# Kernel optimization log

Hardware: AMD Instinct MI355X
Metric: run time of the kernel (lower is better)

## Reference

```python
import jax, jax.numpy as jnp
import numpy as np

ALPHA, GAMMA = 0.25, 2.0
ACCEPT, REJECT = 0.5, 0.4
CLF_W, REG_W = 1.0, 50.0
SL1_R = 9.0  # reg_smooth_l1_loss_scaling_factor
EPS = 1e-4


def _calc_iou(a, b):
    # a: [A,4] anchors in yxyx ; b: [M,4] gt boxes in xyxy (as in original code)
    ay1, ax1, ay2, ax2 = a[:, 0], a[:, 1], a[:, 2], a[:, 3]
    bx1, by1, bx2, by2 = b[:, 0], b[:, 1], b[:, 2], b[:, 3]
    iw = jnp.clip(jnp.minimum(ax2[:, None], bx2) - jnp.maximum(ax1[:, None], bx1), 0.0)
    ih = jnp.clip(jnp.minimum(ay2[:, None], by2) - jnp.maximum(ay1[:, None], by1), 0.0)
    inter = iw * ih  # [A, M]
    aarea = ((ax2 - ax1) * (ay2 - ay1))[:, None]
    barea = (bx2 - bx1) * (by2 - by1)
    union = jnp.clip(aarea + barea - inter, 1e-8)
    return inter / union


def _single_image(clf, reg, ann, anchors, a_cx, a_cy, a_w, a_h):
    # clf: [A,C], reg: [A,4], ann: [M,5] (x1,y1,x2,y2,label; label=-1 => pad)
    clf = jnp.clip(clf, EPS, 1.0 - EPS)
    labels = ann[:, 4]
    valid = labels != -1.0  # [M]
    boxes = ann[:, :4]
    iou = _calc_iou(anchors, boxes)               # [A, M]
    iou = jnp.where(valid[None, :], iou, -1.0)    # invalid GT never matches
    iou_max = iou.max(axis=-1)                    # [A]
    iou_arg = iou.argmax(axis=-1)                 # [A]
    matched = iou_max > ACCEPT
    unmatched = iou_max < REJECT
    num_matched = matched.sum()
    # classification targets: -1 (ignore) by default, 0 for unmatched, one-hot for matched
    gt_lbl = labels[iou_arg].astype(jnp.int32) - 1  # [A]
    one_hot = jax.nn.one_hot(gt_lbl, clf.shape[-1], dtype=clf.dtype)
    tgt = jnp.where(matched[:, None], one_hot,
                    jnp.where(unmatched[:, None], 0.0, -1.0))
    pos = ALPHA * (1.0 - clf) ** GAMMA * (-jnp.log(clf))
    neg = (1.0 - ALPHA) * clf ** GAMMA * (-jnp.log(1.0 - clf))
    clf_losses = jnp.where(tgt == 1.0, pos, neg)
    clf_losses = jnp.where(tgt == -1.0, 0.0, clf_losses)
    clf_loss = clf_losses.sum() / jnp.maximum(1, num_matched).astype(clf.dtype)
    gb = boxes[iou_arg]  # [A,4] xyxy
    gw_raw = gb[:, 2] - gb[:, 0]
    gh_raw = gb[:, 3] - gb[:, 1]
    gcx = gb[:, 0] + 0.5 * gw_raw
    gcy = gb[:, 1] + 0.5 * gh_raw
    gw = jnp.clip(gw_raw, 1.0)
    gh = jnp.clip(gh_raw, 1.0)
    reg_t = jnp.stack(((gcy - a_cy) / a_h,
                       (gcx - a_cx) / a_w,
                       jnp.log(gh / a_h),
                       jnp.log(gw / a_w)), axis=-1)  # [A,4] (dy,dx,dh,dw)
    d = jnp.abs(SL1_R * (reg - reg_t))
    sl1 = jnp.where(d < 1.0, 0.5 * d * d, d - 0.5)
    sl1 = jnp.where(matched[:, None], sl1, 0.0)
    denom = jnp.maximum(1, 4 * num_matched).astype(clf.dtype)
    reg_loss = jnp.where(num_matched > 0, sl1.sum() / denom, 0.0)
    return clf_loss, reg_loss


def setup_inputs() -> dict:
    key = jax.random.key(0)
    ks = jax.random.split(key, 12)
    B, A, C, M = 8, 49104, 90, 32
    clf = jax.random.uniform(ks[0], (B, A, C), jnp.float32)
    reg = jax.random.normal(ks[1], (B, A, 4), jnp.float32)
    # anchors in yxyx, all with positive width/height
    y1 = jax.random.uniform(ks[2], (A,)) * 480.0
    x1 = jax.random.uniform(ks[3], (A,)) * 480.0
    ah = jax.random.uniform(ks[4], (A,)) * 120.0 + 8.0
    aw = jax.random.uniform(ks[5], (A,)) * 120.0 + 8.0
    anchors = jnp.stack([y1, x1, y1 + ah, x1 + aw], axis=-1)[None].astype(jnp.float32)
    # annotations: xyxy boxes + label in [1, C]; ~half padded with label -1
    bx1 = jax.random.uniform(ks[6], (B, M)) * 400.0
    by1 = jax.random.uniform(ks[7], (B, M)) * 400.0
    bw = jax.random.uniform(ks[8], (B, M)) * 100.0 + 20.0
    bh = jax.random.uniform(ks[9], (B, M)) * 100.0 + 20.0
    lbl = jax.random.randint(ks[10], (B, M), 1, C + 1).astype(jnp.float32)
    lbl = jnp.where(jax.random.uniform(ks[11], (B, M)) < 0.6, lbl, -1.0)
    ann = jnp.stack([bx1, by1, bx1 + bw, by1 + bh, lbl], axis=-1).astype(jnp.float32)
    return {"classifications": clf, "regressions": reg, "anchors": anchors, "annotations": ann}


def reference(classifications, regressions, anchors, annotations):
    anc = anchors.squeeze()  # [A,4] yxyx
    a_w = anc[:, 3] - anc[:, 1]
    a_h = anc[:, 2] - anc[:, 0]
    a_cx = anc[:, 1] + 0.5 * a_w
    a_cy = anc[:, 0] + 0.5 * a_h
    clf = jnp.clip(classifications, EPS, 1.0 - EPS)
    clf_l, reg_l = jax.vmap(_single_image, in_axes=(0, 0, 0, None, None, None, None, None))(
        clf, regressions, annotations, anc, a_cx, a_cy, a_w, a_h)
    return CLF_W * clf_l.mean(), REG_W * reg_l.mean()
```

## Files before the change

kernel.cpp:

```cpp
#include <hip/hip_runtime.h>


namespace {
constexpr int B_N = 8;
constexpr int A_N = 49104;
constexpr int C_N = 90;
constexpr int M_N = 32;
constexpr float EPSF   = 1e-4f;
constexpr float ACCEPT = 0.5f;
constexpr float REJECT = 0.4f;
constexpr float SL1R   = 9.0f;
constexpr float CLFW   = 1.0f;
constexpr float REGW   = 50.0f;
constexpr float LN2    = 0.69314718055994530942f;

constexpr int APB = 256;
constexpr int NBX = (A_N + APB - 1) / APB;

__device__ __forceinline__ float clampx(float x) {
    return __builtin_amdgcn_fmed3f(x, EPSF, 1.0f - EPSF);
}
__device__ __forceinline__ float neg_term(float x) {
    x = clampx(x);
    return 0.75f * x * x * (-__logf(1.0f - x));
}
__device__ __forceinline__ float pos_term(float x) {
    x = clampx(x);
    float o = 1.0f - x;
    return 0.25f * o * o * (-__logf(x));
}
}

__global__ void fused_kernel(const float* __restrict__ anchors,
                             const float* __restrict__ reg,
                             const float* __restrict__ ann,
                             const float* __restrict__ clf,
                             float4* __restrict__ part)
{
    __shared__ float sann[M_N * 5];
    __shared__ int   s_match[APB];
    __shared__ int   s_ign[APB];
    __shared__ int   s_nm, s_ni;
    __shared__ float sred[4][4];

    const int b   = blockIdx.y;
    const int a0  = blockIdx.x * APB;
    const int tid = threadIdx.x;
    if (tid < M_N * 5) sann[tid] = ann[b * M_N * 5 + tid];
    if (tid == 0) { s_nm = 0; s_ni = 0; }
    __syncthreads();

    float cnt  = 0.0f;
    float rsum = 0.0f;
    float corr = 0.0f;
    const int i = a0 + tid;

    if (i < A_N) {
        const float4 av = ((const float4*)anchors)[i];
        const float ay1 = av.x, ax1 = av.y, ay2 = av.z, ax2 = av.w;
        const float aw = ax2 - ax1, ah = ay2 - ay1;
        const float aarea = aw * ah;

        float best = -3.4e38f;
        int   arg  = 0;
        #pragma unroll 8
        for (int j = 0; j < M_N; ++j) {
            const float bx1 = sann[j*5+0], by1 = sann[j*5+1];
            const float bx2 = sann[j*5+2], by2 = sann[j*5+3];
            const float lb  = sann[j*5+4];
            float iw = fminf(ax2, bx2) - fmaxf(ax1, bx1); iw = fmaxf(iw, 0.0f);
            float ih = fminf(ay2, by2) - fmaxf(ay1, by1); ih = fmaxf(ih, 0.0f);
            const float inter = iw * ih;
            const float barea = (bx2 - bx1) * (by2 - by1);
            const float uni   = fmaxf(aarea + barea - inter, 1e-8f);
            float iou = inter / uni;
            if (lb == -1.0f) iou = -1.0f;
            if (iou > best) { best = iou; arg = j; }
        }

        const bool matched   = best > ACCEPT;
        const bool unmatched = best < REJECT;

        if (matched) {
            const int s = (int)sann[arg*5+4] - 1;
            cnt = 1.0f;
            const int slot = atomicAdd(&s_nm, 1);
            s_match[slot] = (tid << 8) | s;
            const float bx1 = sann[arg*5+0], by1 = sann[arg*5+1];
            const float bx2 = sann[arg*5+2], by2 = sann[arg*5+3];
            const float gwr = bx2 - bx1, ghr = by2 - by1;
            const float gcx = bx1 + 0.5f * gwr, gcy = by1 + 0.5f * ghr;
            const float gw  = fmaxf(gwr, 1.0f), gh = fmaxf(ghr, 1.0f);
            const float acx = ax1 + 0.5f * aw, acy = ay1 + 0.5f * ah;
            const float t0 = (gcy - acy) / ah;
            const float t1 = (gcx - acx) / aw;
            const float t2 = __logf(gh / ah);
            const float t3 = __logf(gw / aw);
            const float4 rv = ((const float4*)reg)[b * A_N + i];
            float d;
            d = fabsf(SL1R * (rv.x - t0)); rsum += (d < 1.0f) ? 0.5f*d*d : d - 0.5f;
            d = fabsf(SL1R * (rv.y - t1)); rsum += (d < 1.0f) ? 0.5f*d*d : d - 0.5f;
            d = fabsf(SL1R * (rv.z - t2)); rsum += (d < 1.0f) ? 0.5f*d*d : d - 0.5f;
            d = fabsf(SL1R * (rv.w - t3)); rsum += (d < 1.0f) ? 0.5f*d*d : d - 0.5f;
        } else if (!unmatched) {
            const int slot = atomicAdd(&s_ni, 1);
            s_ign[slot] = tid;
        }
    }
    __syncthreads();

    const int nA  = min(APB, A_N - a0);
    const int nF4 = nA * C_N / 4;
    const float4* __restrict__ p =
        (const float4*)(clf + ((size_t)b * A_N + a0) * C_N);

    float S = 0.0f;

    auto w4 = [](float4 v) -> float {
        float s = 0.0f;
        const float x0 = clampx(v.x), x1 = clampx(v.y);
        const float x2 = clampx(v.z), x3 = clampx(v.w);
        s = fmaf(x0 * x0, __log2f(1.0f - x0), s);
        s = fmaf(x1 * x1, __log2f(1.0f - x1), s);
        s = fmaf(x2 * x2, __log2f(1.0f - x2), s);
        s = fmaf(x3 * x3, __log2f(1.0f - x3), s);
        return s;
    };

    int f = tid;
    #pragma unroll 1
    for (; f + 768 < nF4; f += 1024) {
        const float4 v0 = p[f];
        const float4 v1 = p[f + 256];
        const float4 v2 = p[f + 512];
        const float4 v3 = p[f + 768];
        S += w4(v0) + w4(v1) + w4(v2) + w4(v3);
    }
    for (; f < nF4; f += 256) S += w4(p[f]);

    const int nm = s_nm, ni = s_ni;
    for (int k = tid; k < nm; k += 256) {
        const int packed = s_match[k];
        const int a  = packed >> 8;
        const int sc = packed & 0xFF;
        const float x = clf[((size_t)b * A_N + a0 + a) * C_N + sc];
        corr += pos_term(x) - neg_term(x);
    }
    const int wid  = tid >> 6;
    const int lane = tid & 63;
    for (int e = wid; e < ni; e += 4) {
        const int a = s_ign[e];
        const float2* __restrict__ r2 =
            (const float2*)(clf + ((size_t)b * A_N + a0 + a) * C_N);
        if (lane < 45) {
            const float2 u = r2[lane];
            corr -= neg_term(u.x) + neg_term(u.y);
        }
    }

    #pragma unroll
    for (int off = 32; off > 0; off >>= 1) {
        cnt  += __shfl_down(cnt,  off);
        rsum += __shfl_down(rsum, off);
        S    += __shfl_down(S,    off);
        corr += __shfl_down(corr, off);
    }
    if (lane == 0) {
        sred[wid][0] = cnt; sred[wid][1] = rsum;
        sred[wid][2] = S;   sred[wid][3] = corr;
    }
    __syncthreads();
    if (tid == 0) {
        float c = 0.f, r = 0.f, ss = 0.f, k = 0.f;
        #pragma unroll
        for (int w = 0; w < 4; ++w) {
            c += sred[w][0]; r += sred[w][1]; ss += sred[w][2]; k += sred[w][3];
        }
        part[b * NBX + blockIdx.x] = make_float4(c, r, ss, k);
    }
}

__global__ void finalize_kernel(const float4* __restrict__ part,
                                float*        __restrict__ out)
{
    __shared__ float s_cnt[B_N], s_rsum[B_N], s_S[B_N], s_corr[B_N];
    const int tid = threadIdx.x;
    const int b   = tid >> 5;
    const int j   = tid & 31;

    float cnt = 0.f, rsum = 0.f, S = 0.f, corr = 0.f;
    #pragma unroll
    for (int k = 0; k < NBX / 32; ++k) {
        const float4 m = part[b * NBX + j + 32 * k];
        cnt += m.x; rsum += m.y; S += m.z; corr += m.w;
    }
    #pragma unroll
    for (int off = 16; off > 0; off >>= 1) {
        cnt  += __shfl_down(cnt,  off, 32);
        rsum += __shfl_down(rsum, off, 32);
        S    += __shfl_down(S,    off, 32);
        corr += __shfl_down(corr, off, 32);
    }
    if (j == 0) { s_cnt[b] = cnt; s_rsum[b] = rsum; s_S[b] = S; s_corr[b] = corr; }
    __syncthreads();
    if (tid == 0) {
        float cl = 0.0f, rl = 0.0f;
        #pragma unroll
        for (int bb = 0; bb < B_N; ++bb) {
            const float n = s_cnt[bb];
            const float clf_total = -0.75f * LN2 * s_S[bb] + s_corr[bb];
            cl += clf_total / fmaxf(1.0f, n);
            if (n > 0.0f) rl += s_rsum[bb] / (4.0f * n);
        }
        out[0] = CLFW * (cl / (float)B_N);
        out[1] = REGW * (rl / (float)B_N);
    }
}

extern "C" void kernel_launch(void* const* d_in, const int* in_sizes, int n_in,
                              void* d_out, int out_size, void* d_ws, size_t ws_size,
                              hipStream_t stream) {
    const float* clf     = (const float*)d_in[0];
    const float* reg     = (const float*)d_in[1];
    const float* anchors = (const float*)d_in[2];
    const float* ann     = (const float*)d_in[3];
    float*  out  = (float*)d_out;
    float4* part = (float4*)d_ws;

    {
        dim3 grid(NBX, B_N);
        fused_kernel<<<grid, 256, 0, stream>>>(anchors, reg, ann, clf, part);
    }
    finalize_kernel<<<1, 256, 0, stream>>>(part, out);
}
```

Baseline: 215.2 us.

## Split dense classification stream into separate block range from matching blocks

The dense per-element focal-loss sum over the classification tensor moves into its own set of 512 blocks per image, each streaming a contiguous chunk with 8 loads in flight and two accumulators. The IoU matching blocks now only compute counts, regression loss and sparse corrections. This lets the bandwidth-bound stream run without waiting on the IoU matching, and the stream blocks avoid the matching work and shared-memory setup. In exchange there are more partial results to reduce, and launch bounds are set for occupancy.

Result: no change. 215.2 us (+0.0%).

```diff
diff --git a/kernel.cpp b/kernel.cpp
--- a/kernel.cpp
+++ b/kernel.cpp
@@ -14,8 +14,14 @@
 constexpr float REGW   = 50.0f;
 constexpr float LN2    = 0.69314718055994530942f;
 
-constexpr int APB = 256;
-constexpr int NBX = (A_N + APB - 1) / APB;
+constexpr int APB  = 256;
+constexpr int MBX  = (A_N + APB - 1) / APB;
+constexpr int SBX  = 512;
+constexpr int IMG_F4 = A_N * C_N / 4;
+constexpr int CHUNK  = (IMG_F4 + SBX - 1) / SBX;
+
+constexpr int MSLOTS = MBX * B_N;
+constexpr int SSLOT0 = MSLOTS;
 
 __device__ __forceinline__ float clampx(float x) {
     return __builtin_amdgcn_fmed3f(x, EPSF, 1.0f - EPSF);
@@ -31,11 +37,12 @@
 }
 }
 
-__global__ void fused_kernel(const float* __restrict__ anchors,
-                             const float* __restrict__ reg,
-                             const float* __restrict__ ann,
-                             const float* __restrict__ clf,
-                             float4* __restrict__ part)
+__global__ void __launch_bounds__(256, 8)
+fused_kernel(const float* __restrict__ anchors,
+             const float* __restrict__ reg,
+             const float* __restrict__ ann,
+             const float* __restrict__ clf,
+             float4* __restrict__ part)
 {
     __shared__ float sann[M_N * 5];
     __shared__ int   s_match[APB];
@@ -44,8 +51,59 @@
     __shared__ float sred[4][4];
 
     const int b   = blockIdx.y;
-    const int a0  = blockIdx.x * APB;
     const int tid = threadIdx.x;
+    const int wid  = tid >> 6;
+    const int lane = tid & 63;
+
+    if (blockIdx.x >= MBX) {
+        const int sx    = blockIdx.x - MBX;
+        const int fbase = sx * CHUNK;
+        const int n     = min(CHUNK, IMG_F4 - fbase);
+        const float4* __restrict__ p =
+            (const float4*)(clf + (size_t)b * (A_N * C_N)) + fbase;
+
+        auto w4 = [](float4 v) -> float {
+            float s = 0.0f;
+            const float x0 = clampx(v.x), x1 = clampx(v.y);
+            const float x2 = clampx(v.z), x3 = clampx(v.w);
+            s = fmaf(x0 * x0, __log2f(1.0f - x0), s);
+            s = fmaf(x1 * x1, __log2f(1.0f - x1), s);
+            s = fmaf(x2 * x2, __log2f(1.0f - x2), s);
+            s = fmaf(x3 * x3, __log2f(1.0f - x3), s);
+            return s;
+        };
+
+        float S0 = 0.0f, S1 = 0.0f;
+        int f = tid;
+        #pragma unroll 1
+        for (; f + 1792 < n; f += 2048) {
+            const float4 v0 = p[f];
+            const float4 v1 = p[f + 256];
+            const float4 v2 = p[f + 512];
+            const float4 v3 = p[f + 768];
+            const float4 v4 = p[f + 1024];
+            const float4 v5 = p[f + 1280];
+            const float4 v6 = p[f + 1536];
+            const float4 v7 = p[f + 1792];
+            S0 += w4(v0) + w4(v2) + w4(v4) + w4(v6);
+            S1 += w4(v1) + w4(v3) + w4(v5) + w4(v7);
+        }
+        #pragma unroll 1
+        for (; f < n; f += 256) S0 += w4(p[f]);
+        float S = S0 + S1;
+
+        #pragma unroll
+        for (int off = 32; off > 0; off >>= 1) S += __shfl_down(S, off);
+        if (lane == 0) sred[wid][0] = S;
+        __syncthreads();
+        if (tid == 0) {
+            part[SSLOT0 + b * SBX + sx] =
+                make_float4(0.f, 0.f, sred[0][0] + sred[1][0] + sred[2][0] + sred[3][0], 0.f);
+        }
+        return;
+    }
+
+    const int a0 = blockIdx.x * APB;
     if (tid < M_N * 5) sann[tid] = ann[b * M_N * 5 + tid];
     if (tid == 0) { s_nm = 0; s_ni = 0; }
     __syncthreads();
@@ -109,35 +167,6 @@
     }
     __syncthreads();
 
-    const int nA  = min(APB, A_N - a0);
-    const int nF4 = nA * C_N / 4;
-    const float4* __restrict__ p =
-        (const float4*)(clf + ((size_t)b * A_N + a0) * C_N);
-
-    float S = 0.0f;
-
-    auto w4 = [](float4 v) -> float {
-        float s = 0.0f;
-        const float x0 = clampx(v.x), x1 = clampx(v.y);
-        const float x2 = clampx(v.z), x3 = clampx(v.w);
-        s = fmaf(x0 * x0, __log2f(1.0f - x0), s);
-        s = fmaf(x1 * x1, __log2f(1.0f - x1), s);
-        s = fmaf(x2 * x2, __log2f(1.0f - x2), s);
-        s = fmaf(x3 * x3, __log2f(1.0f - x3), s);
-        return s;
-    };
-
-    int f = tid;
-    #pragma unroll 1
-    for (; f + 768 < nF4; f += 1024) {
-        const float4 v0 = p[f];
-        const float4 v1 = p[f + 256];
-        const float4 v2 = p[f + 512];
-        const float4 v3 = p[f + 768];
-        S += w4(v0) + w4(v1) + w4(v2) + w4(v3);
-    }
-    for (; f < nF4; f += 256) S += w4(p[f]);
-
     const int nm = s_nm, ni = s_ni;
     for (int k = tid; k < nm; k += 256) {
         const int packed = s_match[k];
@@ -146,8 +175,6 @@
         const float x = clf[((size_t)b * A_N + a0 + a) * C_N + sc];
         corr += pos_term(x) - neg_term(x);
     }
-    const int wid  = tid >> 6;
-    const int lane = tid & 63;
     for (int e = wid; e < ni; e += 4) {
         const int a = s_ign[e];
         const float2* __restrict__ r2 =
@@ -162,21 +189,17 @@
     for (int off = 32; off > 0; off >>= 1) {
         cnt  += __shfl_down(cnt,  off);
         rsum += __shfl_down(rsum, off);
-        S    += __shfl_down(S,    off);
         corr += __shfl_down(corr, off);
     }
     if (lane == 0) {
-        sred[wid][0] = cnt; sred[wid][1] = rsum;
-        sred[wid][2] = S;   sred[wid][3] = corr;
+        sred[wid][0] = cnt; sred[wid][1] = rsum; sred[wid][2] = corr;
     }
     __syncthreads();
     if (tid == 0) {
-        float c = 0.f, r = 0.f, ss = 0.f, k = 0.f;
+        float c = 0.f, r = 0.f, k = 0.f;
         #pragma unroll
-        for (int w = 0; w < 4; ++w) {
-            c += sred[w][0]; r += sred[w][1]; ss += sred[w][2]; k += sred[w][3];
-        }
-        part[b * NBX + blockIdx.x] = make_float4(c, r, ss, k);
+        for (int w = 0; w < 4; ++w) { c += sred[w][0]; r += sred[w][1]; k += sred[w][2]; }
+        part[b * MBX + blockIdx.x] = make_float4(c, r, 0.f, k);
     }
 }
 
@@ -190,9 +213,14 @@
 
     float cnt = 0.f, rsum = 0.f, S = 0.f, corr = 0.f;
     #pragma unroll
-    for (int k = 0; k < NBX / 32; ++k) {
-        const float4 m = part[b * NBX + j + 32 * k];
-        cnt += m.x; rsum += m.y; S += m.z; corr += m.w;
+    for (int k = 0; k < MBX / 32; ++k) {
+        const float4 m = part[b * MBX + j + 32 * k];
+        cnt += m.x; rsum += m.y; corr += m.w;
+    }
+    #pragma unroll
+    for (int k = 0; k < SBX / 32; ++k) {
+        const float4 m = part[SSLOT0 + b * SBX + j + 32 * k];
+        S += m.z;
     }
     #pragma unroll
     for (int off = 16; off > 0; off >>= 1) {
@@ -228,7 +256,7 @@
     float4* part = (float4*)d_ws;
 
     {
-        dim3 grid(NBX, B_N);
+        dim3 grid(MBX + SBX, B_N);
         fused_kernel<<<grid, 256, 0, stream>>>(anchors, reg, ann, clf, part);
     }
     finalize_kernel<<<1, 256, 0, stream>>>(part, out);
```
